# Performance work log

Measured on AMD Instinct MI355X. Metric: run time of the kernel, lower is better.

## Reference

```python
import jax, jax.numpy as jnp
import numpy as np

B, T, D = 2, 4096, 2048
H, K = 16, 128          # num_heads, head_dim (V == K)
P = H * K               # projection size
C = 64                  # chunk_size
CONV = 4                # conv_size
LAT = 128               # snapshot_latent_dim
CPS = 256 // C          # chunks_per_snapshot
EPS = 1e-6


def _silu(x):
    return x * jax.nn.sigmoid(x)


def _dwconv_silu(x, w):
    # causal depthwise conv1d: x (B,T,P), w (P,CONV)
    y = jax.lax.conv_general_dilated(
        x.transpose(0, 2, 1), w[:, None, :], (1,), [(w.shape[-1] - 1, 0)],
        feature_group_count=x.shape[-1], dimension_numbers=('NCH', 'OIH', 'NCH'))
    return _silu(y.transpose(0, 2, 1))


def _rmsnorm(x, w, eps=EPS):
    return x * jax.lax.rsqrt(jnp.mean(x * x, axis=-1, keepdims=True) + eps) * w


def _l2norm(x):
    return x * jax.lax.rsqrt(jnp.sum(x * x, axis=-1, keepdims=True) + 1e-12)


def setup_inputs() -> dict:
    key = jax.random.key(0)
    ks = jax.random.split(key, 20)
    sD, sK = D ** -0.5, K ** -0.5
    return {
        'x': jax.random.normal(ks[0], (B, T, D), jnp.float32),
        'Wq': jax.random.normal(ks[1], (P, D), jnp.float32) * sD,
        'Wk': jax.random.normal(ks[2], (P, D), jnp.float32) * sD,
        'Wv': jax.random.normal(ks[3], (P, D), jnp.float32) * sD,
        'conv_q': jax.random.normal(ks[4], (P, CONV), jnp.float32) * 0.5,
        'conv_k': jax.random.normal(ks[5], (P, CONV), jnp.float32) * 0.5,
        'conv_v': jax.random.normal(ks[6], (P, CONV), jnp.float32) * 0.5,
        'A_log': jnp.log(jax.random.uniform(ks[7], (H,), jnp.float32, 1.0, 8.0)),
        'dt_bias': jax.random.normal(ks[8], (P,), jnp.float32) * 0.1 - 3.0,
        'Wfa': jax.random.normal(ks[9], (K, D), jnp.float32) * sD,
        'Wfb': jax.random.normal(ks[10], (P, K), jnp.float32) * sK,
        'Wb': jax.random.normal(ks[11], (H, D), jnp.float32) * sD,
        'Wga': jax.random.normal(ks[12], (K, D), jnp.float32) * sD,
        'Wgb': jax.random.normal(ks[13], (P, K), jnp.float32) * sK,
        'bgb': jnp.zeros((P,), jnp.float32),
        'o_norm_w': jnp.ones((K,), jnp.float32),
        'Wo': jax.random.normal(ks[14], (D, P), jnp.float32) * (P ** -0.5),
        'snap_norm_w': jnp.ones((K * K,), jnp.float32),
        'snap_down': jax.random.normal(ks[15], (LAT, K * K), jnp.float32) * (K ** -1.0),
    }


def _forward(x, Wq, Wk, Wv, conv_q, conv_k, conv_v, A_log, dt_bias, Wfa, Wfb,
             Wb, Wga, Wgb, bgb, o_norm_w, Wo, snap_norm_w, snap_down):
    Bx, Tx, _ = x.shape
    Nc = Tx // C
    # projections + short causal conv + silu
    q = _dwconv_silu(x @ Wq.T, conv_q).reshape(Bx, Tx, H, K)
    k = _dwconv_silu(x @ Wk.T, conv_k).reshape(Bx, Tx, H, K)
    v = _dwconv_silu(x @ Wv.T, conv_v).reshape(Bx, Tx, H, K)
    # KDA gate: log forget gate per (t, h, k)
    g_raw = (x @ Wfa.T) @ Wfb.T                               # (B,T,P)
    log_g = (-jnp.exp(A_log))[None, None, :, None] * \
        jax.nn.softplus(g_raw + dt_bias).reshape(Bx, Tx, H, K)
    beta = jax.nn.sigmoid(x @ Wb.T)                           # (B,T,H)
    # qk l2-norm + scale
    q = _l2norm(q) * (K ** -0.5)
    k = _l2norm(k)
    # chunk: (B,T,H,K) -> (B,H,Nc,C,K)
    def ch(a):
        return a.reshape(Bx, Nc, C, H, -1).transpose(0, 3, 1, 2, 4)
    qc, kc, vc, gc = ch(q), ch(k), ch(v), ch(log_g)
    bc = beta.reshape(Bx, Nc, C, H).transpose(0, 3, 1, 2)     # (B,H,Nc,C)
    cum = jnp.maximum(jnp.cumsum(gc, axis=-2), -15.0)
    Wg = jnp.exp(cum)
    Wi = jnp.exp(-cum)
    u_mat = kc * Wi
    w_mat = kc * Wg
    q_tilde = qc * Wg
    be = bc[..., None]
    bw = be * w_mat
    bv = be * vc
    L = jnp.tril(jnp.einsum('bhnik,bhnjk->bhnij', bw, u_mat), -1)
    A_mat = L + jnp.eye(C, dtype=L.dtype)
    ev = jax.lax.linalg.triangular_solve(A_mat, bv, left_side=True, lower=True, unit_diagonal=True)
    ew = jax.lax.linalg.triangular_solve(A_mat, bw, left_side=True, lower=True, unit_diagonal=True)
    intra = jnp.tril(jnp.einsum('bhnik,bhnjk->bhnij', q_tilde, u_mat), 0)
    w_last = Wg[..., -1, :]                                   # (B,H,Nc,K)

    def body(S, inp):
        qt_n, um_n, ev_n, ew_n, ia_n, wl_n = inp
        delta = ev_n - ew_n @ S                               # (B,H,C,V)
        o_n = qt_n @ S + ia_n @ delta
        S_new = wl_n[..., None] * (S + jnp.einsum('bhck,bhcv->bhkv', um_n, delta))
        return S_new, (o_n, S_new)

    xs = tuple(jnp.moveaxis(a, 2, 0) for a in (q_tilde, u_mat, ev, ew, intra, w_last))
    S0 = jnp.zeros((Bx, H, K, K), jnp.float32)
    _, (o_chunks, S_all) = jax.lax.scan(body, S0, xs)
    out = o_chunks.transpose(1, 0, 3, 2, 4).reshape(Bx, Tx, H, K)
    # compressed snapshots every CPS chunks
    S_snap = S_all[CPS - 1::CPS]                              # (Ns,B,H,K,K)
    Ns = S_snap.shape[0]
    flat = S_snap.reshape(Ns, Bx, H, K * K)
    snaps = (_rmsnorm(flat, snap_norm_w) @ snap_down.T).transpose(1, 0, 2, 3)  # (B,Ns,H,LAT)
    # gated output norm + output projection
    gate = ((x @ Wga.T) @ Wgb.T + bgb).reshape(Bx, Tx, H, K)
    o = _rmsnorm(out, o_norm_w) * jax.nn.sigmoid(gate)
    y = o.reshape(Bx, Tx, P) @ Wo.T
    return y, snaps


def reference(x, Wq, Wk, Wv, conv_q, conv_k, conv_v, A_log, dt_bias, Wfa, Wfb,
              Wb, Wga, Wgb, bgb, o_norm_w, Wo, snap_norm_w, snap_down):
    return _forward(x, Wq, Wk, Wv, conv_q, conv_k, conv_v, A_log, dt_bias,
                    Wfa, Wfb, Wb, Wga, Wgb, bgb, o_norm_w, Wo,
                    snap_norm_w, snap_down)
```

## Files before the change

kernel.cpp:

```cpp
#include <hip/hip_runtime.h>

constexpr int Bc   = 2;
constexpr int Tc   = 4096;
constexpr int Dc   = 2048;
constexpr int Hc   = 16;
constexpr int Kc   = 128;
constexpr int Pc   = Hc * Kc;
constexpr int Cc   = 64;
constexpr int NCc  = Tc / Cc;
constexpr int Mc   = Bc * Tc;
constexpr int LATc = 128;

__device__ __forceinline__ float bf2f(unsigned short u) {
  unsigned int x = ((unsigned int)u) << 16;
  return __builtin_bit_cast(float, x);
}
__device__ __forceinline__ unsigned short f2bf(float f) {
  unsigned int x = __builtin_bit_cast(unsigned int, f);
  x += 0x7fffu + ((x >> 16) & 1u);
  return (unsigned short)(x >> 16);
}
__device__ __forceinline__ float4 ld4(const float* p) {
  return *reinterpret_cast<const float4*>(p);
}
__device__ __forceinline__ float4 ld4(const unsigned short* p) {
  ushort4 u = *reinterpret_cast<const ushort4*>(p);
  return make_float4(bf2f(u.x), bf2f(u.y), bf2f(u.z), bf2f(u.w));
}
__device__ __forceinline__ void st1(float* p, float v) { *p = v; }
__device__ __forceinline__ void st1(unsigned short* p, float v) { *p = f2bf(v); }

__device__ __forceinline__ float fsig(float x) {
  return __fdividef(1.f, 1.f + __expf(-x));
}
__device__ __forceinline__ float fsoftplus(float g) {
  return (g > 20.f) ? g : __logf(1.f + __expf(g));
}

typedef __attribute__((ext_vector_type(8))) short bf16x8;
typedef __attribute__((ext_vector_type(4))) float f32x4;

__device__ __forceinline__ int swzA(int row, int kbyte) { return row * 256 + (kbyte ^ ((row & 7) << 4)); }
__device__ __forceinline__ int swzB(int row, int kbyte) { return row * 128 + (kbyte ^ ((row & 7) << 4)); }
__device__ __forceinline__ int swzC(int row, int kbyte) { return row * 64 + (kbyte ^ (((row >> 2) & 3) << 4)); }
__device__ __forceinline__ bf16x8 ldsv8(const unsigned short* base, int byteoff) {
  return *reinterpret_cast<const bf16x8*>(reinterpret_cast<const char*>(base) + byteoff);
}
__device__ __forceinline__ void stsv16B(unsigned short* base, int byteoff, int4 v) {
  *reinterpret_cast<int4*>(reinterpret_cast<char*>(base) + byteoff) = v;
}
__device__ __forceinline__ void stsv8B(unsigned short* base, int byteoff, uint2 v) {
  *reinterpret_cast<uint2*>(reinterpret_cast<char*>(base) + byteoff) = v;
}
__device__ __forceinline__ unsigned short lds16(const unsigned short* base, int byteoff) {
  return *reinterpret_cast<const unsigned short*>(reinterpret_cast<const char*>(base) + byteoff);
}

__device__ __forceinline__ int xcd_swz(int id, int nwg) {
  if ((nwg & 7) != 0 || nwg < 16) return id;
  return (id & 7) * (nwg >> 3) + (id >> 3);
}

__global__ void cast_f32_bf16(const float* __restrict__ in, unsigned short* __restrict__ out,
                              int n) {
  int i = (blockIdx.x * 256 + threadIdx.x) * 4;
  if (i < n) {
    float4 v = ld4(in + i);
    ushort4 o;
    o.x = f2bf(v.x); o.y = f2bf(v.y); o.z = f2bf(v.z); o.w = f2bf(v.w);
    *reinterpret_cast<ushort4*>(out + i) = o;
  }
}

__device__ __forceinline__ void gload_lds16(const unsigned short* g, unsigned short* l) {
  __builtin_amdgcn_global_load_lds(
      (const __attribute__((address_space(1))) void*)g,
      (__attribute__((address_space(3))) void*)l, 16, 0, 0);
}

__device__ __forceinline__ void tile_map(int& m0, int& n0) {
  int id = blockIdx.y * gridDim.x + blockIdx.x;
  id = xcd_swz(id, gridDim.x * gridDim.y);
  const int bpg = gridDim.y << 3;
  int grp = id / bpg, rem = id % bpg;
  m0 = ((grp << 3) + (rem & 7)) * 128;
  n0 = (rem >> 3) * 128;
}

template <typename OT>
__global__ __launch_bounds__(256) void gemm_nt_mfma(const unsigned short* __restrict__ A,
                                                    const unsigned short* __restrict__ Bm,
                                                    OT* __restrict__ Out,
                                                    int Ndim, int Kd) {
  __shared__ __align__(16) unsigned short As[128 * 32];
  __shared__ __align__(16) unsigned short Bs[128 * 32];
  int m0, n0;
  tile_map(m0, n0);
  const int tid = threadIdx.x;
  const int wave = tid >> 6;
  const int lane = tid & 63;
  const int wr = wave >> 1, wc = wave & 1;
  const int l15 = lane & 15, l4 = lane >> 4;
  const int kxor = (l4 ^ ((l15 >> 1) & 3)) << 3;
  f32x4 acc[4][4] = {};

  for (int k0 = 0; k0 < Kd; k0 += 32) {
#pragma unroll
    for (int i = 0; i < 2; ++i) {
      int slot = (wave * 2 + i) * 64 + lane;
      int r = slot >> 2;
      int kg = (slot & 3) ^ ((r >> 1) & 3);
      gload_lds16(&A[(size_t)(m0 + r) * Kd + k0 + kg * 8], &As[(wave * 2 + i) * 512]);
      gload_lds16(&Bm[(size_t)(n0 + r) * Kd + k0 + kg * 8], &Bs[(wave * 2 + i) * 512]);
    }
    __syncthreads();
    bf16x8 af[4], bfr[4];
#pragma unroll
    for (int m = 0; m < 4; ++m)
      af[m] = *reinterpret_cast<const bf16x8*>(&As[(wr * 64 + m * 16 + l15) * 32 + kxor]);
#pragma unroll
    for (int n = 0; n < 4; ++n)
      bfr[n] = *reinterpret_cast<const bf16x8*>(&Bs[(wc * 64 + n * 16 + l15) * 32 + kxor]);
#pragma unroll
    for (int m = 0; m < 4; ++m)
#pragma unroll
      for (int n = 0; n < 4; ++n)
        acc[m][n] = __builtin_amdgcn_mfma_f32_16x16x32_bf16(af[m], bfr[n], acc[m][n], 0, 0, 0);
    __syncthreads();
  }
#pragma unroll
  for (int m = 0; m < 4; ++m)
#pragma unroll
    for (int n = 0; n < 4; ++n)
#pragma unroll
      for (int r = 0; r < 4; ++r) {
        int row = m0 + wr * 64 + m * 16 + l4 * 4 + r;
        int col = n0 + wc * 64 + n * 16 + l15;
        st1(&Out[(size_t)row * Ndim + col], acc[m][n][r]);
      }
}

__global__ __launch_bounds__(256) void gemm_nt_mfma_qkv(const unsigned short* __restrict__ A,
                                                        const unsigned short* __restrict__ Bm,
                                                        unsigned short* __restrict__ Out,
                                                        int Kd) {
  __shared__ __align__(16) unsigned short As[128 * 32];
  __shared__ __align__(16) unsigned short Bs[128 * 32];
  int m0, n0;
  tile_map(m0, n0);
  const int tid = threadIdx.x;
  const int wave = tid >> 6;
  const int lane = tid & 63;
  const int wr = wave >> 1, wc = wave & 1;
  const int l15 = lane & 15, l4 = lane >> 4;
  const int kxor = (l4 ^ ((l15 >> 1) & 3)) << 3;
  f32x4 acc[4][4] = {};

  for (int k0 = 0; k0 < Kd; k0 += 32) {
#pragma unroll
    for (int i = 0; i < 2; ++i) {
      int slot = (wave * 2 + i) * 64 + lane;
      int r = slot >> 2;
      int kg = (slot & 3) ^ ((r >> 1) & 3);
      gload_lds16(&A[(size_t)(m0 + r) * Kd + k0 + kg * 8], &As[(wave * 2 + i) * 512]);
      gload_lds16(&Bm[(size_t)(n0 + r) * Kd + k0 + kg * 8], &Bs[(wave * 2 + i) * 512]);
    }
    __syncthreads();
    bf16x8 af[4], bfr[4];
#pragma unroll
    for (int m = 0; m < 4; ++m)
      af[m] = *reinterpret_cast<const bf16x8*>(&As[(wr * 64 + m * 16 + l15) * 32 + kxor]);
#pragma unroll
    for (int n = 0; n < 4; ++n)
      bfr[n] = *reinterpret_cast<const bf16x8*>(&Bs[(wc * 64 + n * 16 + l15) * 32 + kxor]);
#pragma unroll
    for (int m = 0; m < 4; ++m)
#pragma unroll
      for (int n = 0; n < 4; ++n)
        acc[m][n] = __builtin_amdgcn_mfma_f32_16x16x32_bf16(af[m], bfr[n], acc[m][n], 0, 0, 0);
    __syncthreads();
  }
  unsigned short* dst = Out + (size_t)(n0 >> 11) * ((size_t)Mc * 2048);
  const int cbase = n0 & 2047;
#pragma unroll
  for (int m = 0; m < 4; ++m)
#pragma unroll
    for (int n = 0; n < 4; ++n)
#pragma unroll
      for (int r = 0; r < 4; ++r) {
        int row = m0 + wr * 64 + m * 16 + l4 * 4 + r;
        int col = cbase + wc * 64 + n * 16 + l15;
        dst[(size_t)row * 2048 + col] = f2bf(acc[m][n][r]);
      }
}

__global__ __launch_bounds__(256) void gemm_nt_mfma_fgb(const unsigned short* __restrict__ A,
                                                        const unsigned short* __restrict__ Bm,
                                                        unsigned short* __restrict__ fab,
                                                        unsigned short* __restrict__ gab,
                                                        unsigned short* __restrict__ betabb,
                                                        int Kd) {
  __shared__ __align__(16) unsigned short As[128 * 32];
  __shared__ __align__(16) unsigned short Bs[128 * 32];
  int m0, n0;
  tile_map(m0, n0);
  const int tid = threadIdx.x;
  const int wave = tid >> 6;
  const int lane = tid & 63;
  const int wr = wave >> 1, wc = wave & 1;
  const int l15 = lane & 15, l4 = lane >> 4;
  const int kxor = (l4 ^ ((l15 >> 1) & 3)) << 3;
  f32x4 acc[4][4] = {};

  for (int k0 = 0; k0 < Kd; k0 += 32) {
#pragma unroll
    for (int i = 0; i < 2; ++i) {
      int slot = (wave * 2 + i) * 64 + lane;
      int r = slot >> 2;
      int kg = (slot & 3) ^ ((r >> 1) & 3);
      gload_lds16(&A[(size_t)(m0 + r) * Kd + k0 + kg * 8], &As[(wave * 2 + i) * 512]);
      gload_lds16(&Bm[(size_t)(n0 + r) * Kd + k0 + kg * 8], &Bs[(wave * 2 + i) * 512]);
    }
    __syncthreads();
    bf16x8 af[4], bfr[4];
#pragma unroll
    for (int m = 0; m < 4; ++m)
      af[m] = *reinterpret_cast<const bf16x8*>(&As[(wr * 64 + m * 16 + l15) * 32 + kxor]);
#pragma unroll
    for (int n = 0; n < 4; ++n)
      bfr[n] = *reinterpret_cast<const bf16x8*>(&Bs[(wc * 64 + n * 16 + l15) * 32 + kxor]);
#pragma unroll
    for (int m = 0; m < 4; ++m)
#pragma unroll
      for (int n = 0; n < 4; ++n)
        acc[m][n] = __builtin_amdgcn_mfma_f32_16x16x32_bf16(af[m], bfr[n], acc[m][n], 0, 0, 0);
    __syncthreads();
  }
  unsigned short* dst = (n0 == 0) ? fab : ((n0 == 128) ? gab : betabb);
#pragma unroll
  for (int m = 0; m < 4; ++m)
#pragma unroll
    for (int n = 0; n < 4; ++n)
#pragma unroll
      for (int r = 0; r < 4; ++r) {
        int row = m0 + wr * 64 + m * 16 + l4 * 4 + r;
        int lc = wc * 64 + n * 16 + l15;
        dst[(size_t)row * 128 + lc] = f2bf(acc[m][n][r]);
      }
}

__global__ __launch_bounds__(256) void gemm_nt_mfma_sk(const unsigned short* __restrict__ A,
                                                       const unsigned short* __restrict__ Bm,
                                                       float* __restrict__ Part,
                                                       int Ndim, int Kd, int kslice, int Mtot) {
  __shared__ __align__(16) unsigned short As[128 * 32];
  __shared__ __align__(16) unsigned short Bs[128 * 32];
  const int m0 = blockIdx.x * 128;
  const int n0 = blockIdx.y * 128;
  const int kz = blockIdx.z * kslice;
  const int tid = threadIdx.x;
  const int wave = tid >> 6;
  const int lane = tid & 63;
  const int wr = wave >> 1, wc = wave & 1;
  const int l15 = lane & 15, l4 = lane >> 4;
  const int kxor = (l4 ^ ((l15 >> 1) & 3)) << 3;
  f32x4 acc[4][4] = {};

  for (int k0 = kz; k0 < kz + kslice; k0 += 32) {
#pragma unroll
    for (int i = 0; i < 2; ++i) {
      int slot = (wave * 2 + i) * 64 + lane;
      int r = slot >> 2;
      int kg = (slot & 3) ^ ((r >> 1) & 3);
      gload_lds16(&A[(size_t)(m0 + r) * Kd + k0 + kg * 8], &As[(wave * 2 + i) * 512]);
      gload_lds16(&Bm[(size_t)(n0 + r) * Kd + k0 + kg * 8], &Bs[(wave * 2 + i) * 512]);
    }
    __syncthreads();
    bf16x8 af[4], bfr[4];
#pragma unroll
    for (int m = 0; m < 4; ++m)
      af[m] = *reinterpret_cast<const bf16x8*>(&As[(wr * 64 + m * 16 + l15) * 32 + kxor]);
#pragma unroll
    for (int n = 0; n < 4; ++n)
      bfr[n] = *reinterpret_cast<const bf16x8*>(&Bs[(wc * 64 + n * 16 + l15) * 32 + kxor]);
#pragma unroll
    for (int m = 0; m < 4; ++m)
#pragma unroll
      for (int n = 0; n < 4; ++n)
        acc[m][n] = __builtin_amdgcn_mfma_f32_16x16x32_bf16(af[m], bfr[n], acc[m][n], 0, 0, 0);
    __syncthreads();
  }
  float* out = Part + (size_t)blockIdx.z * Mtot * Ndim;
#pragma unroll
  for (int m = 0; m < 4; ++m)
#pragma unroll
    for (int n = 0; n < 4; ++n)
#pragma unroll
      for (int r = 0; r < 4; ++r) {
        int row = m0 + wr * 64 + m * 16 + l4 * 4 + r;
        int col = n0 + wc * 64 + n * 16 + l15;
        out[(size_t)row * Ndim + col] = acc[m][n][r];
      }
}

__global__ __launch_bounds__(256) void chunk_prep(
    const unsigned short* __restrict__ q_lin, const unsigned short* __restrict__ k_lin,
    const unsigned short* __restrict__ v_lin, const unsigned short* __restrict__ g_raw,
    const unsigned short* __restrict__ beta16, const float* __restrict__ conv_q,
    const float* __restrict__ conv_k, const float* __restrict__ conv_v,
    const float* __restrict__ A_log, const float* __restrict__ dt_bias,
    unsigned short* __restrict__ qt, unsigned short* __restrict__ u_,
    unsigned short* __restrict__ bv, unsigned short* __restrict__ bw,
    float* __restrict__ wlast) {
  const int wave = threadIdx.x >> 6, lane = threadIdx.x & 63;
  const int cid = blockIdx.x * 4 + wave;
  const int n = cid & 63;
  const int h = (cid >> 6) & 15;
  const int b = cid >> 10;
  const int k0 = 2 * lane;
  const int p = h * Kc + k0;
  float cq[2][4], ck[2][4], cv[2][4];
#pragma unroll
  for (int s = 0; s < 2; ++s)
#pragma unroll
    for (int j = 0; j < 4; ++j) {
      cq[s][j] = conv_q[(p + s) * 4 + j];
      ck[s][j] = conv_k[(p + s) * 4 + j];
      cv[s][j] = conv_v[(p + s) * 4 + j];
    }
  const float aneg = -__expf(A_log[h]);
  const float db0 = dt_bias[p], db1 = dt_bias[p + 1];
  float cum0 = 0.f, cum1 = 0.f;
  const int t0 = n * Cc;
  float wq[2][3] = {}, wk[2][3] = {}, wv[2][3] = {};
#pragma unroll
  for (int d = 0; d < 3; ++d) {
    int ts = t0 - 3 + d;
    if (ts >= 0) {
      size_t o = ((size_t)(b * Tc + ts)) * Pc + p;
      ushort2 q2 = *(const ushort2*)(q_lin + o);
      ushort2 k2 = *(const ushort2*)(k_lin + o);
      ushort2 v2 = *(const ushort2*)(v_lin + o);
      wq[0][d] = bf2f(q2.x); wq[1][d] = bf2f(q2.y);
      wk[0][d] = bf2f(k2.x); wk[1][d] = bf2f(k2.y);
      wv[0][d] = bf2f(v2.x); wv[1][d] = bf2f(v2.y);
    }
  }
  for (int c = 0; c < Cc; ++c) {
    const int t = t0 + c;
    size_t off = ((size_t)(b * Tc + t)) * Pc + p;
    ushort2 q2 = *(const ushort2*)(q_lin + off);
    ushort2 k2 = *(const ushort2*)(k_lin + off);
    ushort2 v2 = *(const ushort2*)(v_lin + off);
    ushort2 g2 = *(const ushort2*)(g_raw + off);
    float nq[2] = {bf2f(q2.x), bf2f(q2.y)};
    float nk[2] = {bf2f(k2.x), bf2f(k2.y)};
    float nv[2] = {bf2f(v2.x), bf2f(v2.y)};
    float qv[2], kv[2], vv[2];
#pragma unroll
    for (int s = 0; s < 2; ++s) {
      qv[s] = cq[s][0] * wq[s][0] + cq[s][1] * wq[s][1] + cq[s][2] * wq[s][2] + cq[s][3] * nq[s];
      kv[s] = ck[s][0] * wk[s][0] + ck[s][1] * wk[s][1] + ck[s][2] * wk[s][2] + ck[s][3] * nk[s];
      vv[s] = cv[s][0] * wv[s][0] + cv[s][1] * wv[s][1] + cv[s][2] * wv[s][2] + cv[s][3] * nv[s];
      wq[s][0] = wq[s][1]; wq[s][1] = wq[s][2]; wq[s][2] = nq[s];
      wk[s][0] = wk[s][1]; wk[s][1] = wk[s][2]; wk[s][2] = nk[s];
      wv[s][0] = wv[s][1]; wv[s][1] = wv[s][2]; wv[s][2] = nv[s];
      qv[s] = qv[s] * fsig(qv[s]);
      kv[s] = kv[s] * fsig(kv[s]);
      vv[s] = vv[s] * fsig(vv[s]);
    }
    float a = qv[0] * qv[0] + qv[1] * qv[1];
    float bb = kv[0] * kv[0] + kv[1] * kv[1];
#pragma unroll
    for (int off2 = 32; off2 > 0; off2 >>= 1) {
      a += __shfl_xor(a, off2, 64);
      bb += __shfl_xor(bb, off2, 64);
    }
    float rq = rsqrtf(a + 1e-12f) * 0.08838834764831845f;
    float rk = rsqrtf(bb + 1e-12f);
    float g0 = bf2f(g2.x) + db0, g1 = bf2f(g2.y) + db1;
    cum0 += aneg * fsoftplus(g0);
    cum1 += aneg * fsoftplus(g1);
    float cc0 = fmaxf(cum0, -15.f), cc1 = fmaxf(cum1, -15.f);
    float Wg0 = __expf(cc0), Wg1 = __expf(cc1);
    float Wi0 = __fdividef(1.f, Wg0), Wi1 = __fdividef(1.f, Wg1);
    float beta = fsig(bf2f(beta16[((size_t)(b * Tc + t)) * 128 + h]));
    size_t idx = ((size_t)cid * Cc + c) * Kc + k0;
    ushort2 o1, o2, o3, o4;
    o1.x = f2bf(qv[0] * rq * Wg0); o1.y = f2bf(qv[1] * rq * Wg1);
    o2.x = f2bf(kv[0] * rk * Wi0); o2.y = f2bf(kv[1] * rk * Wi1);
    o3.x = f2bf(beta * kv[0] * rk * Wg0); o3.y = f2bf(beta * kv[1] * rk * Wg1);
    o4.x = f2bf(beta * vv[0]); o4.y = f2bf(beta * vv[1]);
    *(ushort2*)(qt + idx) = o1;
    *(ushort2*)(u_ + idx) = o2;
    *(ushort2*)(bw + idx) = o3;
    *(ushort2*)(bv + idx) = o4;
    if (c == Cc - 1) {
      wlast[(size_t)cid * Kc + k0] = Wg0;
      wlast[(size_t)cid * Kc + k0 + 1] = Wg1;
    }
  }
}

__global__ __launch_bounds__(256) void chunk_solve_mfma(
    const unsigned short* __restrict__ qt, unsigned short* __restrict__ u_,
    unsigned short* __restrict__ evb,
    unsigned short* __restrict__ ewb,
    unsigned short* __restrict__ intra_out) {
  const int blk = blockIdx.x;
  const size_t base = (size_t)blk * (Cc * Kc);
  const size_t ibase = (size_t)blk * (Cc * Cc);
  const int tid = threadIdx.x, wave = tid >> 6, lane = tid & 63;
  const int l15 = lane & 15, l4 = lane >> 4;

  __shared__ __align__(16) char lds[65536];
  unsigned short* uS   = (unsigned short*)(lds);
  unsigned short* qtS  = (unsigned short*)(lds + 16384);
  unsigned short* bwS  = (unsigned short*)(lds + 32768);
  unsigned short* NLrm = (unsigned short*)(lds + 49152);
  unsigned short* NLT  = (unsigned short*)(lds + 57344);
  unsigned short* Trm  = (unsigned short*)(lds);
  unsigned short* TT   = (unsigned short*)(lds + 8192);
  unsigned short* Prm  = (unsigned short*)(lds + 16384);
  unsigned short* PT   = (unsigned short*)(lds + 24576);
  unsigned short* bvT  = (unsigned short*)(lds + 32768);
  unsigned short* bwT  = (unsigned short*)(lds + 49152);

#pragma unroll
  for (int i = 0; i < 4; ++i) {
    int cid = tid + i * 256;
    int r = cid >> 4, c8 = (cid & 15) * 8, cb2 = (cid & 15) * 16;
    int4 vu = *(const int4*)(u_ + base + (size_t)r * 128 + c8);
    int4 vb = *(const int4*)(ewb + base + (size_t)r * 128 + c8);
    int4 vq = *(const int4*)(qt + base + (size_t)r * 128 + c8);
    stsv16B(uS, swzA(r, cb2), vu);
    stsv16B(bwS, swzA(r, cb2), vb);
    stsv16B(qtS, swzA(r, cb2), vq);
  }
  __syncthreads();

  const int arow = 16 * wave + l15;
  bf16x8 aBw[4], aQt[4];
#pragma unroll
  for (int ks = 0; ks < 4; ++ks) {
    aBw[ks] = ldsv8(bwS, swzA(arow, 16 * l4 + 64 * ks));
    aQt[ks] = ldsv8(qtS, swzA(arow, 16 * l4 + 64 * ks));
  }
  f32x4 Lc[4], Ic[4];
#pragma unroll
  for (int nt = 0; nt < 4; ++nt) {
    f32x4 a = {}, bq = {};
#pragma unroll
    for (int ks = 0; ks < 4; ++ks) {
      bf16x8 bu = ldsv8(uS, swzA(16 * nt + l15, 16 * l4 + 64 * ks));
      a = __builtin_amdgcn_mfma_f32_16x16x32_bf16(aBw[ks], bu, a, 0, 0, 0);
      bq = __builtin_amdgcn_mfma_f32_16x16x32_bf16(aQt[ks], bu, bq, 0, 0, 0);
    }
    Lc[nt] = a; Ic[nt] = bq;
  }
#pragma unroll
  for (int nt = 0; nt < 4; ++nt)
#pragma unroll
    for (int r = 0; r < 4; ++r) {
      int row = 16 * wave + 4 * l4 + r, col = 16 * nt + l15;
      intra_out[ibase + (size_t)row * 64 + col] = f2bf((col <= row) ? Ic[nt][r] : 0.f);
    }

#pragma unroll
  for (int i = 0; i < 4; ++i) {
    int w2 = tid + i * 256;
    int k = w2 >> 3, cg = w2 & 7;
    unsigned short tmp[8];
#pragma unroll
    for (int j = 0; j < 8; ++j) {
      int c = cg + 8 * j;
      tmp[j] = lds16(uS, swzA(c, 2 * k));
    }
#pragma unroll
    for (int j = 0; j < 8; ++j)
      u_[base + (size_t)k * 64 + cg + 8 * j] = tmp[j];
  }
  __syncthreads();

  f32x4 Tf[4];
#pragma unroll
  for (int nt = 0; nt < 4; ++nt)
#pragma unroll
    for (int r = 0; r < 4; ++r) {
      int row = 16 * wave + 4 * l4 + r, col = 16 * nt + l15;
      float nl = (col < row) ? -Lc[nt][r] : 0.f;
      unsigned short nb = f2bf(nl);
      *reinterpret_cast<unsigned short*>((char*)NLrm + swzB(row, col * 2)) = nb;
      *reinterpret_cast<unsigned short*>((char*)NLT + swzB(col, row * 2)) = nb;
      float t0 = nl + ((row == col) ? 1.f : 0.f);
      Tf[nt][r] = t0;
      unsigned short tb = f2bf(t0);
      *reinterpret_cast<unsigned short*>((char*)Trm + swzB(row, col * 2)) = tb;
      *reinterpret_cast<unsigned short*>((char*)TT + swzB(col, row * 2)) = tb;
    }
  __syncthreads();

  bf16x8 aN[2];
#pragma unroll
  for (int ks = 0; ks < 2; ++ks) aN[ks] = ldsv8(NLrm, swzB(arow, 16 * l4 + 64 * ks));
  f32x4 Pf[4];
#pragma unroll
  for (int nt = 0; nt < 4; ++nt) {
    f32x4 acc = {};
#pragma unroll
    for (int ks = 0; ks < 2; ++ks)
      acc = __builtin_amdgcn_mfma_f32_16x16x32_bf16(aN[ks], ldsv8(NLT, swzB(16 * nt + l15, 16 * l4 + 64 * ks)), acc, 0, 0, 0);
    Pf[nt] = acc;
  }
  int4 rv[4], rw[4];
#pragma unroll
  for (int i = 0; i < 4; ++i) {
    int cid = tid + i * 256;
    int r = cid >> 4, c8 = (cid & 15) * 8;
    rv[i] = *(const int4*)(evb + base + (size_t)r * 128 + c8);
    rw[i] = *(const int4*)(ewb + base + (size_t)r * 128 + c8);
  }
#pragma unroll
  for (int nt = 0; nt < 4; ++nt)
#pragma unroll
    for (int r = 0; r < 4; ++r) {
      int row = 16 * wave + 4 * l4 + r, col = 16 * nt + l15;
      unsigned short pb = f2bf(Pf[nt][r]);
      *reinterpret_cast<unsigned short*>((char*)Prm + swzB(row, col * 2)) = pb;
      *reinterpret_cast<unsigned short*>((char*)PT + swzB(col, row * 2)) = pb;
    }
  __syncthreads();

  for (int it = 0; it < 5; ++it) {
    bf16x8 aP[2];
#pragma unroll
    for (int ks = 0; ks < 2; ++ks) aP[ks] = ldsv8(Prm, swzB(arow, 16 * l4 + 64 * ks));
    f32x4 Tn[4], Pn[4];
#pragma unroll
    for (int nt = 0; nt < 4; ++nt) {
      f32x4 acc = Tf[nt];
#pragma unroll
      for (int ks = 0; ks < 2; ++ks)
        acc = __builtin_amdgcn_mfma_f32_16x16x32_bf16(aP[ks], ldsv8(TT, swzB(16 * nt + l15, 16 * l4 + 64 * ks)), acc, 0, 0, 0);
      Tn[nt] = acc;
    }
    if (it < 4) {
#pragma unroll
      for (int nt = 0; nt < 4; ++nt) {
        f32x4 acc = {};
#pragma unroll
        for (int ks = 0; ks < 2; ++ks)
          acc = __builtin_amdgcn_mfma_f32_16x16x32_bf16(aP[ks], ldsv8(PT, swzB(16 * nt + l15, 16 * l4 + 64 * ks)), acc, 0, 0, 0);
        Pn[nt] = acc;
      }
    }
    __syncthreads();
#pragma unroll
    for (int nt = 0; nt < 4; ++nt)
#pragma unroll
      for (int r = 0; r < 4; ++r) {
        int row = 16 * wave + 4 * l4 + r, col = 16 * nt + l15;
        unsigned short tb = f2bf(Tn[nt][r]);
        *reinterpret_cast<unsigned short*>((char*)Trm + swzB(row, col * 2)) = tb;
        *reinterpret_cast<unsigned short*>((char*)TT + swzB(col, row * 2)) = tb;
        if (it < 4) {
          unsigned short pb = f2bf(Pn[nt][r]);
          *reinterpret_cast<unsigned short*>((char*)Prm + swzB(row, col * 2)) = pb;
          *reinterpret_cast<unsigned short*>((char*)PT + swzB(col, row * 2)) = pb;
        }
      }
#pragma unroll
    for (int nt = 0; nt < 4; ++nt) Tf[nt] = Tn[nt];
    __syncthreads();
  }

#pragma unroll
  for (int i = 0; i < 4; ++i) {
    int cid = tid + i * 256;
    int r = cid >> 4;
    const unsigned short* pv = reinterpret_cast<const unsigned short*>(&rv[i]);
    const unsigned short* pw = reinterpret_cast<const unsigned short*>(&rw[i]);
#pragma unroll
    for (int j = 0; j < 8; ++j) {
      int v = (cid & 15) * 8 + j;
      *reinterpret_cast<unsigned short*>((char*)bvT + swzB(v, r * 2)) = pv[j];
      *reinterpret_cast<unsigned short*>((char*)bwT + swzB(v, r * 2)) = pw[j];
    }
  }
  __syncthreads();

  bf16x8 aT[2];
#pragma unroll
  for (int ks = 0; ks < 2; ++ks) aT[ks] = ldsv8(Trm, swzB(arow, 16 * l4 + 64 * ks));
#pragma unroll
  for (int nt = 0; nt < 8; ++nt) {
    f32x4 e = {}, w2 = {};
#pragma unroll
    for (int ks = 0; ks < 2; ++ks) {
      e = __builtin_amdgcn_mfma_f32_16x16x32_bf16(aT[ks], ldsv8(bvT, swzB(16 * nt + l15, 16 * l4 + 64 * ks)), e, 0, 0, 0);
      w2 = __builtin_amdgcn_mfma_f32_16x16x32_bf16(aT[ks], ldsv8(bwT, swzB(16 * nt + l15, 16 * l4 + 64 * ks)), w2, 0, 0, 0);
    }
#pragma unroll
    for (int r = 0; r < 4; ++r) {
      int row = 16 * wave + 4 * l4 + r, col = 16 * nt + l15;
      evb[base + (size_t)row * 128 + col] = f2bf(e[r]);
      ewb[base + (size_t)row * 128 + col] = f2bf(w2[r]);
    }
  }
}

__global__ __launch_bounds__(512) void scan_mfma(
    const unsigned short* __restrict__ qt, const unsigned short* __restrict__ uT,
    const unsigned short* __restrict__ evb, const unsigned short* __restrict__ ewb,
    const unsigned short* __restrict__ intra, const float* __restrict__ wlast,
    unsigned short* __restrict__ attn_o, unsigned short* __restrict__ snapb) {
  const int id = xcd_swz(blockIdx.x, 128);
  const int bh = id >> 2, vs = id & 3;
  const int b = bh >> 4, h = bh & 15;
  const int v0 = vs * 32;
  const int tid = threadIdx.x, wave = tid >> 6, lane = tid & 63;
  const int l15 = lane & 15, l4 = lane >> 4;
  __shared__ __align__(16) unsigned short ewS[8192];
  __shared__ __align__(16) unsigned short qtS[8192];
  __shared__ __align__(16) unsigned short uTS[8192];
  __shared__ __align__(16) unsigned short iaS[4096];
  __shared__ __align__(16) unsigned short evS[2048];
  __shared__ __align__(16) unsigned short sBT[4096];
  __shared__ __align__(16) unsigned short dBT[2048];

  f32x4 S[2] = {};
  {
    int4 z = {0, 0, 0, 0};
    stsv16B(sBT, tid * 16, z);
  }

  const int sr = tid >> 3;
  const int sk0 = (tid & 7) * 16;
  const int sc0 = (tid & 7) * 8;
  const int evc = (tid & 7) * 4;
  const int tk = tid >> 3;
  const int wloff = 16 * wave + 4 * l4;
  int4 rEw0, rEw1, rQt0, rQt1, rUT0, rUT1, rIa;
  uint2 rEv;
  float4 rWlN, rWlC;

#define STAGE_LOAD(CB, IB, NN)                                                    \
  rEw0 = *(const int4*)(ewb + (CB) + sr * 128 + sk0);                             \
  rEw1 = *(const int4*)(ewb + (CB) + sr * 128 + sk0 + 8);                         \
  rQt0 = *(const int4*)(qt + (CB) + sr * 128 + sk0);                              \
  rQt1 = *(const int4*)(qt + (CB) + sr * 128 + sk0 + 8);                          \
  rEv = *(const uint2*)(evb + (CB) + sr * 128 + v0 + evc);                        \
  rUT0 = *(const int4*)(uT + (CB) + (size_t)tk * 64 + sc0);                       \
  rUT1 = *(const int4*)(uT + (CB) + (size_t)(tk + 64) * 64 + sc0);                \
  rIa = *(const int4*)(intra + (IB) + sr * 64 + sc0);                             \
  rWlN = ld4(wlast + ((size_t)bh * 64 + (NN)) * 128 + wloff);

#define STAGE_WRITE()                                                             \
  stsv16B(ewS, swzA(sr, sk0 * 2), rEw0);                                          \
  stsv16B(ewS, swzA(sr, sk0 * 2 + 16), rEw1);                                     \
  stsv16B(qtS, swzA(sr, sk0 * 2), rQt0);                                          \
  stsv16B(qtS, swzA(sr, sk0 * 2 + 16), rQt1);                                     \
  stsv8B(evS, swzC(sr, evc * 2), rEv);                                            \
  stsv16B(iaS, swzB(sr, sc0 * 2), rIa);                                           \
  stsv16B(uTS, swzB(tk, sc0 * 2), rUT0);                                          \
  stsv16B(uTS, swzB(tk + 64, sc0 * 2), rUT1);

  {
    const size_t cb0 = (size_t)bh * 64 * 8192;
    const size_t ib0 = (size_t)bh * 64 * 4096;
    STAGE_LOAD(cb0, ib0, 0);
    STAGE_WRITE();
    rWlC = rWlN;
  }
  __syncthreads();

  const int m = wave & 3, vg = wave >> 2;
  const int arow = 16 * m + l15;
  const int krow = 16 * wave + l15;
  const int vl = 16 * vg + l15;

  for (int n = 0; n < NCc; ++n) {
    const size_t cb = ((size_t)bh * 64 + n) * 8192;
    const size_t ib = ((size_t)bh * 64 + n) * 4096;
    if (n < 63) { STAGE_LOAD(cb + 8192, ib + 4096, n + 1); }
    bf16x8 aEw[4];
#pragma unroll
    for (int ks = 0; ks < 4; ++ks) aEw[ks] = ldsv8(ewS, swzA(arow, 16 * l4 + 64 * ks));
    {
      f32x4 p = {};
#pragma unroll
      for (int ks = 0; ks < 4; ++ks)
        p = __builtin_amdgcn_mfma_f32_16x16x32_bf16(aEw[ks], ldsv8(sBT, swzA(vl, 16 * l4 + 64 * ks)), p, 0, 0, 0);
      float d[4];
#pragma unroll
      for (int r = 0; r < 4; ++r) {
        int c = 16 * m + 4 * l4 + r;
        d[r] = bf2f(lds16(evS, swzC(c, 2 * vl))) - p[r];
      }
      uint2 pk;
      pk.x = (unsigned)f2bf(d[0]) | ((unsigned)f2bf(d[1]) << 16);
      pk.y = (unsigned)f2bf(d[2]) | ((unsigned)f2bf(d[3]) << 16);
      stsv8B(dBT, swzB(vl, (16 * m + 4 * l4) * 2), pk);
    }
    __syncthreads();
    bf16x8 aQt[4], aIa[2], aU[2];
#pragma unroll
    for (int ks = 0; ks < 4; ++ks) aQt[ks] = ldsv8(qtS, swzA(arow, 16 * l4 + 64 * ks));
#pragma unroll
    for (int ks = 0; ks < 2; ++ks) aIa[ks] = ldsv8(iaS, swzB(arow, 16 * l4 + 64 * ks));
#pragma unroll
    for (int ks = 0; ks < 2; ++ks) aU[ks] = ldsv8(uTS, swzB(krow, 16 * l4 + 64 * ks));
    {
      f32x4 o = {};
#pragma unroll
      for (int ks = 0; ks < 4; ++ks)
        o = __builtin_amdgcn_mfma_f32_16x16x32_bf16(aQt[ks], ldsv8(sBT, swzA(vl, 16 * l4 + 64 * ks)), o, 0, 0, 0);
#pragma unroll
      for (int ks = 0; ks < 2; ++ks)
        o = __builtin_amdgcn_mfma_f32_16x16x32_bf16(aIa[ks], ldsv8(dBT, swzB(vl, 16 * l4 + 64 * ks)), o, 0, 0, 0);
#pragma unroll
      for (int r = 0; r < 4; ++r) {
        int c = 16 * m + 4 * l4 + r;
        int t = n * 64 + c;
        attn_o[((size_t)(b * Tc + t) * Hc + h) * Kc + v0 + vl] = f2bf(o[r]);
      }
    }
    float wlv[4] = {rWlC.x, rWlC.y, rWlC.z, rWlC.w};
#pragma unroll
    for (int vt2 = 0; vt2 < 2; ++vt2) {
      int vl2 = 16 * vt2 + l15;
      f32x4 U = {};
#pragma unroll
      for (int ks = 0; ks < 2; ++ks)
        U = __builtin_amdgcn_mfma_f32_16x16x32_bf16(aU[ks], ldsv8(dBT, swzB(vl2, 16 * l4 + 64 * ks)), U, 0, 0, 0);
#pragma unroll
      for (int r = 0; r < 4; ++r) S[vt2][r] = wlv[r] * (S[vt2][r] + U[r]);
    }
    __syncthreads();
#pragma unroll
    for (int vt2 = 0; vt2 < 2; ++vt2) {
      int vl2 = 16 * vt2 + l15;
      uint2 pk;
      pk.x = (unsigned)f2bf(S[vt2][0]) | ((unsigned)f2bf(S[vt2][1]) << 16);
      pk.y = (unsigned)f2bf(S[vt2][2]) | ((unsigned)f2bf(S[vt2][3]) << 16);
      stsv8B(sBT, swzA(vl2, (16 * wave + 4 * l4) * 2), pk);
    }
    if (n < 63) { STAGE_WRITE(); rWlC = rWlN; }
    if ((n & 3) == 3) {
      int ns = n >> 2;
      size_t sb = (size_t)((ns * Bc + b) * Hc + h) * 16384;
#pragma unroll
      for (int vt2 = 0; vt2 < 2; ++vt2)
#pragma unroll
        for (int r = 0; r < 4; ++r) {
          int k = 16 * wave + 4 * l4 + r;
          snapb[sb + (size_t)k * 128 + v0 + 16 * vt2 + l15] = f2bf(S[vt2][r]);
        }
    }
    __syncthreads();
  }
#undef STAGE_LOAD
#undef STAGE_WRITE
}

__global__ void sdw_mul_bf16(const float* __restrict__ snap_down, const float* __restrict__ w,
                             unsigned short* __restrict__ sdwb) {
  int i = (blockIdx.x * 256 + threadIdx.x) * 4;
  float4 v = ld4(snap_down + i);
  int k = i & 16383;
  float4 ww = ld4(w + k);
  ushort4 o;
  o.x = f2bf(v.x * ww.x); o.y = f2bf(v.y * ww.y); o.z = f2bf(v.z * ww.z); o.w = f2bf(v.w * ww.w);
  *reinterpret_cast<ushort4*>(sdwb + i) = o;
}

__global__ __launch_bounds__(256) void snap_scale_kernel(const unsigned short* __restrict__ snapb,
                                                         float* __restrict__ scale) {
  int r = blockIdx.x;
  const unsigned short* row = snapb + (size_t)r * 16384;
  float s = 0.f;
  for (int ii = threadIdx.x * 4; ii < 16384; ii += 1024) {
    float4 x = ld4(row + ii);
    s += x.x * x.x + x.y * x.y + x.z * x.z + x.w * x.w;
  }
#pragma unroll
  for (int off = 32; off > 0; off >>= 1) s += __shfl_down(s, off, 64);
  __shared__ float red[4];
  if ((threadIdx.x & 63) == 0) red[threadIdx.x >> 6] = s;
  __syncthreads();
  if (threadIdx.x == 0) {
    float tot = red[0] + red[1] + red[2] + red[3];
    scale[r] = rsqrtf(tot * (1.f / 16384.f) + 1e-6f);
  }
}

__global__ void snap_reduce_scatter(const float* __restrict__ part,
                                    const float* __restrict__ scale,
                                    float* __restrict__ outp) {
  int idx = blockIdx.x * 256 + threadIdx.x;
  int l = idx & 127;
  int hh = (idx >> 7) & 15;
  int ns = (idx >> 11) & 15;
  int bb = idx >> 15;
  int r = (ns * Bc + bb) * Hc + hh;
  float s = 0.f;
#pragma unroll
  for (int z = 0; z < 16; ++z) s += part[(size_t)z * 65536 + r * 128 + l];
  outp[idx] = s * scale[r];
}

__global__ __launch_bounds__(256) void out_norm_gate(unsigned short* __restrict__ attn_io,
                                                     const unsigned short* __restrict__ gate_raw,
                                                     const float* __restrict__ bgb,
                                                     const float* __restrict__ o_norm_w) {
  const int wave = threadIdx.x >> 6, lane = threadIdx.x & 63;
  const int blk = blockIdx.x * 4 + wave;
  const int h = blk & 15;
  const size_t row = (size_t)(blk >> 4);
  const size_t base = (size_t)blk * Kc;
  ushort2 xv = *reinterpret_cast<const ushort2*>(attn_io + base + 2 * lane);
  float x0 = bf2f(xv.x), x1 = bf2f(xv.y);
  float ss = x0 * x0 + x1 * x1;
#pragma unroll
  for (int off = 32; off > 0; off >>= 1) ss += __shfl_xor(ss, off, 64);
  float inv = rsqrtf(ss * (1.f / 128.f) + 1e-6f);
  const int p0 = h * Kc + 2 * lane;
  ushort2 gv = *reinterpret_cast<const ushort2*>(gate_raw + row * Pc + p0);
  float g0 = bf2f(gv.x) + bgb[p0];
  float g1 = bf2f(gv.y) + bgb[p0 + 1];
  float o0 = x0 * inv * o_norm_w[2 * lane] * fsig(g0);
  float o1 = x1 * inv * o_norm_w[2 * lane + 1] * fsig(g1);
  ushort2 ov; ov.x = f2bf(o0); ov.y = f2bf(o1);
  *reinterpret_cast<ushort2*>(attn_io + base + 2 * lane) = ov;
}

extern "C" void kernel_launch(void* const* d_in, const int* in_sizes, int n_in,
                              void* d_out, int out_size, void* d_ws, size_t ws_size,
                              hipStream_t stream) {
  (void)in_sizes; (void)n_in;
  const float* x        = (const float*)d_in[0];
  const float* Wq       = (const float*)d_in[1];
  const float* Wk       = (const float*)d_in[2];
  const float* Wv       = (const float*)d_in[3];
  const float* conv_q   = (const float*)d_in[4];
  const float* conv_k   = (const float*)d_in[5];
  const float* conv_v   = (const float*)d_in[6];
  const float* A_log    = (const float*)d_in[7];
  const float* dt_bias  = (const float*)d_in[8];
  const float* Wfa      = (const float*)d_in[9];
  const float* Wfb      = (const float*)d_in[10];
  const float* Wb       = (const float*)d_in[11];
  const float* Wga      = (const float*)d_in[12];
  const float* Wgb      = (const float*)d_in[13];
  const float* bgb      = (const float*)d_in[14];
  const float* o_norm_w = (const float*)d_in[15];
  const float* Wo       = (const float*)d_in[16];
  const float* snap_nw  = (const float*)d_in[17];
  const float* snap_down= (const float*)d_in[18];

  const size_t MP2 = (size_t)Mc * Pc * 2;
  const size_t NEED = 6 * MP2
                    + 2 * (size_t)Mc * Kc * 4
                    + (size_t)Mc * Hc * 4
                    + (size_t)Bc * Hc * NCc * Kc * 4;
  if (ws_size < NEED + 4096) {
    hipMemsetAsync(d_out, 0, (size_t)out_size * 4, stream);
    return;
  }
  char* w = (char*)d_ws;
  auto alloc = [&](size_t bytes) {
    char* r = w;
    w += (bytes + 255) & ~(size_t)255;
    return r;
  };
  unsigned short* q_lin = (unsigned short*)alloc(MP2);
  unsigned short* k_lin = (unsigned short*)alloc(MP2);
  unsigned short* v_lin = (unsigned short*)alloc(MP2);
  unsigned short* g_raw = (unsigned short*)alloc(MP2);
  unsigned short* evb   = (unsigned short*)alloc(MP2);
  unsigned short* ewb   = (unsigned short*)alloc(MP2);
  float* fa    = (float*)alloc((size_t)Mc * Kc * 4);
  float* ga    = (float*)alloc((size_t)Mc * Kc * 4);
  float* betab = (float*)alloc((size_t)Mc * Hc * 4);
  float* wlast = (float*)alloc((size_t)Bc * Hc * NCc * Kc * 4);
  (void)betab;

  unsigned short* qt = (unsigned short*)d_out;
  unsigned short* u_ = (unsigned short*)((char*)d_out + MP2);

  unsigned short* xb    = evb;
  unsigned short* Wqb   = ewb;
  unsigned short* Wkb   = ewb + 4194304;
  unsigned short* Wvb   = ewb + 8388608;
  unsigned short* Wfab  = ewb + 12582912;
  unsigned short* Wgab  = ewb + 12845056;
  unsigned short* Wbp   = ewb + 13107200;
  unsigned short* Wfbb  = ewb + 13369344;
  unsigned short* fab   = (unsigned short*)fa;
  unsigned short* betabb= (unsigned short*)fa + 1048576;
  unsigned short* gab   = (unsigned short*)ga;

  unsigned short* intra = q_lin;
  unsigned short* Wob   = q_lin + 8388608;
  unsigned short* Wgbb  = q_lin + 12582912;
  unsigned short* attn  = k_lin;
  unsigned short* gate_raw = g_raw;
  unsigned short* snapb = v_lin;
  unsigned short* sdwb  = v_lin + (size_t)512 * 16384;
  float* partial   = (float*)ewb;
  float* snapscale = (float*)(ewb + 4400000);

  float* y = (float*)d_out;
  float* snaps_out = (float*)d_out + (size_t)Bc * Tc * Dc;

  cast_f32_bf16<<<16384, 256, 0, stream>>>(x, xb, Mc * Dc);
  cast_f32_bf16<<<4096, 256, 0, stream>>>(Wq, Wqb, Pc * Dc);
  cast_f32_bf16<<<4096, 256, 0, stream>>>(Wk, Wkb, Pc * Dc);
  cast_f32_bf16<<<4096, 256, 0, stream>>>(Wv, Wvb, Pc * Dc);
  cast_f32_bf16<<<256, 256, 0, stream>>>(Wfa, Wfab, Kc * Dc);
  cast_f32_bf16<<<256, 256, 0, stream>>>(Wga, Wgab, Kc * Dc);
  hipMemsetAsync(Wbp, 0, (size_t)128 * 2048 * 2, stream);
  cast_f32_bf16<<<32, 256, 0, stream>>>(Wb, Wbp, Hc * Dc);
  cast_f32_bf16<<<256, 256, 0, stream>>>(Wfb, Wfbb, Pc * Kc);

  gemm_nt_mfma_qkv<<<dim3(64, 48), 256, 0, stream>>>(xb, Wqb, q_lin, Dc);
  gemm_nt_mfma_fgb<<<dim3(64, 3), 256, 0, stream>>>(xb, Wfab, fab, gab, betabb, Dc);
  gemm_nt_mfma<unsigned short><<<dim3(64, 16), 256, 0, stream>>>(fab, Wfbb, g_raw, Pc, Kc);

  chunk_prep<<<Bc * Hc * NCc / 4, 256, 0, stream>>>(q_lin, k_lin, v_lin, g_raw, betabb, conv_q,
                                                    conv_k, conv_v, A_log, dt_bias, qt, u_, evb,
                                                    ewb, wlast);

  cast_f32_bf16<<<4096, 256, 0, stream>>>(Wo, Wob, Dc * Pc);
  cast_f32_bf16<<<256, 256, 0, stream>>>(Wgb, Wgbb, Pc * Kc);

  chunk_solve_mfma<<<Bc * Hc * NCc, 256, 0, stream>>>(qt, u_, evb, ewb, intra);

  gemm_nt_mfma<unsigned short><<<dim3(64, 16), 256, 0, stream>>>(gab, Wgbb, gate_raw, Pc, Kc);

  scan_mfma<<<Bc * Hc * 4, 512, 0, stream>>>(qt, u_, evb, ewb, intra, wlast, attn, snapb);

  sdw_mul_bf16<<<2048, 256, 0, stream>>>(snap_down, snap_nw, sdwb);
  snap_scale_kernel<<<512, 256, 0, stream>>>(snapb, snapscale);
  gemm_nt_mfma_sk<<<dim3(4, 1, 16), 256, 0, stream>>>(snapb, sdwb, partial, 128, 16384, 1024, 512);
  snap_reduce_scatter<<<256, 256, 0, stream>>>(partial, snapscale, snaps_out);

  out_norm_gate<<<Mc * Hc / 4, 256, 0, stream>>>(attn, gate_raw, bgb, o_norm_w);
  gemm_nt_mfma<float><<<dim3(64, 16), 256, 0, stream>>>(attn, Wob, y, Dc, Pc);
}
```

Measured before the change: 858.8 us.

## Split each chunk across four waves with a shared-memory prefix of gate sums

chunk_prep used to give each wave a whole 64-step chunk, walking it serially. Each chunk now gets its own block, and each of the four waves handles 16 timesteps. A first pass computes the softplus gate terms, and per-wave partial sums are exchanged through LDS to seed each wave's cumulative decay. This gives four times more parallelism and a shorter serial dependency chain, at the cost of a block barrier, 32 extra registers for the cached softplus values, and three extra loads of the conv window per wave.

Result: no change. 872.3 us (+1.6%).

```diff
diff --git a/kernel.cpp b/kernel.cpp
--- a/kernel.cpp
+++ b/kernel.cpp
@@ -313,7 +313,7 @@
     unsigned short* __restrict__ bv, unsigned short* __restrict__ bw,
     float* __restrict__ wlast) {
   const int wave = threadIdx.x >> 6, lane = threadIdx.x & 63;
-  const int cid = blockIdx.x * 4 + wave;
+  const int cid = blockIdx.x;
   const int n = cid & 63;
   const int h = (cid >> 6) & 15;
   const int b = cid >> 10;
@@ -330,12 +330,36 @@
     }
   const float aneg = -__expf(A_log[h]);
   const float db0 = dt_bias[p], db1 = dt_bias[p + 1];
-  float cum0 = 0.f, cum1 = 0.f;
-  const int t0 = n * Cc;
+  const int tw = n * Cc + 16 * wave;
+
+  float sp0[16], sp1[16];
+  float ls0 = 0.f, ls1 = 0.f;
+#pragma unroll
+  for (int c = 0; c < 16; ++c) {
+    size_t off = ((size_t)(b * Tc + tw + c)) * Pc + p;
+    ushort2 g2 = *(const ushort2*)(g_raw + off);
+    sp0[c] = fsoftplus(bf2f(g2.x) + db0);
+    sp1[c] = fsoftplus(bf2f(g2.y) + db1);
+    ls0 += sp0[c];
+    ls1 += sp1[c];
+  }
+  __shared__ float part[4][128];
+  part[wave][k0] = ls0;
+  part[wave][k0 + 1] = ls1;
+  __syncthreads();
+  float off0 = 0.f, off1 = 0.f;
+#pragma unroll
+  for (int w2 = 0; w2 < 3; ++w2)
+    if (w2 < wave) {
+      off0 += part[w2][k0];
+      off1 += part[w2][k0 + 1];
+    }
+  float cum0 = aneg * off0, cum1 = aneg * off1;
+
   float wq[2][3] = {}, wk[2][3] = {}, wv[2][3] = {};
 #pragma unroll
   for (int d = 0; d < 3; ++d) {
-    int ts = t0 - 3 + d;
+    int ts = tw - 3 + d;
     if (ts >= 0) {
       size_t o = ((size_t)(b * Tc + ts)) * Pc + p;
       ushort2 q2 = *(const ushort2*)(q_lin + o);
@@ -346,13 +370,14 @@
       wv[0][d] = bf2f(v2.x); wv[1][d] = bf2f(v2.y);
     }
   }
-  for (int c = 0; c < Cc; ++c) {
-    const int t = t0 + c;
+
+#pragma unroll
+  for (int c = 0; c < 16; ++c) {
+    const int t = tw + c;
     size_t off = ((size_t)(b * Tc + t)) * Pc + p;
     ushort2 q2 = *(const ushort2*)(q_lin + off);
     ushort2 k2 = *(const ushort2*)(k_lin + off);
     ushort2 v2 = *(const ushort2*)(v_lin + off);
-    ushort2 g2 = *(const ushort2*)(g_raw + off);
     float nq[2] = {bf2f(q2.x), bf2f(q2.y)};
     float nk[2] = {bf2f(k2.x), bf2f(k2.y)};
     float nv[2] = {bf2f(v2.x), bf2f(v2.y)};
@@ -378,14 +403,13 @@
     }
     float rq = rsqrtf(a + 1e-12f) * 0.08838834764831845f;
     float rk = rsqrtf(bb + 1e-12f);
-    float g0 = bf2f(g2.x) + db0, g1 = bf2f(g2.y) + db1;
-    cum0 += aneg * fsoftplus(g0);
-    cum1 += aneg * fsoftplus(g1);
+    cum0 += aneg * sp0[c];
+    cum1 += aneg * sp1[c];
     float cc0 = fmaxf(cum0, -15.f), cc1 = fmaxf(cum1, -15.f);
     float Wg0 = __expf(cc0), Wg1 = __expf(cc1);
     float Wi0 = __fdividef(1.f, Wg0), Wi1 = __fdividef(1.f, Wg1);
     float beta = fsig(bf2f(beta16[((size_t)(b * Tc + t)) * 128 + h]));
-    size_t idx = ((size_t)cid * Cc + c) * Kc + k0;
+    size_t idx = ((size_t)cid * Cc + (16 * wave + c)) * Kc + k0;
     ushort2 o1, o2, o3, o4;
     o1.x = f2bf(qv[0] * rq * Wg0); o1.y = f2bf(qv[1] * rq * Wg1);
     o2.x = f2bf(kv[0] * rk * Wi0); o2.y = f2bf(kv[1] * rk * Wi1);
@@ -395,7 +419,7 @@
     *(ushort2*)(u_ + idx) = o2;
     *(ushort2*)(bw + idx) = o3;
     *(ushort2*)(bv + idx) = o4;
-    if (c == Cc - 1) {
+    if (wave == 3 && c == 15) {
       wlast[(size_t)cid * Kc + k0] = Wg0;
       wlast[(size_t)cid * Kc + k0 + 1] = Wg1;
     }
@@ -927,9 +951,9 @@
   gemm_nt_mfma_fgb<<<dim3(64, 3), 256, 0, stream>>>(xb, Wfab, fab, gab, betabb, Dc);
   gemm_nt_mfma<unsigned short><<<dim3(64, 16), 256, 0, stream>>>(fab, Wfbb, g_raw, Pc, Kc);
 
-  chunk_prep<<<Bc * Hc * NCc / 4, 256, 0, stream>>>(q_lin, k_lin, v_lin, g_raw, betabb, conv_q,
-                                                    conv_k, conv_v, A_log, dt_bias, qt, u_, evb,
-                                                    ewb, wlast);
+  chunk_prep<<<Bc * Hc * NCc, 256, 0, stream>>>(q_lin, k_lin, v_lin, g_raw, betabb, conv_q,
+                                                conv_k, conv_v, A_log, dt_bias, qt, u_, evb,
+                                                ewb, wlast);
 
   cast_f32_bf16<<<4096, 256, 0, stream>>>(Wo, Wob, Dc * Pc);
   cast_f32_bf16<<<256, 256, 0, stream>>>(Wgb, Wgbb, Pc * Kc);
```
